# Optimization experiments

Hardware: AMD Instinct MI355X
Metric: run time of the kernel (lower is better)

Reference implementation:

```python
import jax, jax.numpy as jnp
import numpy as np

B, S, D, H, DF, L, V, MAXLEN = 8, 1024, 768, 12, 3072, 6, 32000, 2048
HD = D // H
EPS = 1e-5

def _pe(max_length, d_model):
    position = jnp.arange(max_length, dtype=jnp.float32)[:, None]
    i = jnp.arange(d_model, dtype=jnp.float32)[None, :]
    angles = position * (1.0 / jnp.power(10000.0, 2.0 * jnp.floor(i / 2.0) / d_model))
    pe = jnp.zeros((max_length, d_model), dtype=jnp.float32)
    pe = pe.at[:, 0::2].set(jnp.sin(angles[:, 0::2]))
    pe = pe.at[:, 1::2].set(jnp.cos(angles[:, 1::2]))
    return pe

def _layernorm(x, g, b):
    mu = jnp.mean(x, axis=-1, keepdims=True)
    var = jnp.mean((x - mu) ** 2, axis=-1, keepdims=True)
    return (x - mu) * jax.lax.rsqrt(var + EPS) * g + b

def setup_inputs() -> dict:
    key = jax.random.key(0)
    ks = jax.random.split(key, 16)
    s = 0.02
    emb = jax.random.normal(ks[0], (V, D), jnp.float32) * s
    emb = emb.at[0].set(0.0)  # padding_idx=0
    inp = {
        'input_ids': jax.random.randint(ks[1], (B, S), 0, V),
        'emb': emb,
        'pe': _pe(MAXLEN, D),
        'Wq': jax.random.normal(ks[2], (L, D, D), jnp.float32) * s,
        'bq': jnp.zeros((L, D), jnp.float32),
        'Wk': jax.random.normal(ks[3], (L, D, D), jnp.float32) * s,
        'bk': jnp.zeros((L, D), jnp.float32),
        'Wv': jax.random.normal(ks[4], (L, D, D), jnp.float32) * s,
        'bv': jnp.zeros((L, D), jnp.float32),
        'W1': jax.random.normal(ks[5], (L, DF, D), jnp.float32) * s,
        'b1': jnp.zeros((L, DF), jnp.float32),
        'W2': jax.random.normal(ks[6], (L, D, DF), jnp.float32) * s,
        'b2': jnp.zeros((L, D), jnp.float32),
        'ln1_g': jnp.ones((L, D), jnp.float32),
        'ln1_b': jnp.zeros((L, D), jnp.float32),
        'ln2_g': jnp.ones((L, D), jnp.float32),
        'ln2_b': jnp.zeros((L, D), jnp.float32),
    }
    return inp

def _mha(x, Wq, bq, Wk, bk, Wv, bv):
    b, s, _ = x.shape
    q = (x @ Wq.T + bq).reshape(b, H, s, HD)  # faithful to torch .view (no transpose)
    k = (x @ Wk.T + bk).reshape(b, H, s, HD)
    v = (x @ Wv.T + bv).reshape(b, H, s, HD)
    scores = jnp.einsum('bhqd,bhkd->bhqk', q, k) / (HD ** 0.5)
    att = jax.nn.softmax(scores, axis=-1)
    o = jnp.einsum('bhqk,bhkd->bhqd', att, v)
    return o.transpose(0, 2, 1, 3).reshape(b, s, D)

def reference(input_ids, emb, pe, Wq, bq, Wk, bk, Wv, bv, W1, b1, W2, b2, ln1_g, ln1_b, ln2_g, ln2_b):
    x = emb[input_ids] + pe[:input_ids.shape[1], :]
    # dropout is identity in eval mode
    for l in range(L):
        h1 = _mha(x, Wq[l], bq[l], Wk[l], bk[l], Wv[l], bv[l])
        y1 = _layernorm(x + h1, ln1_g[l], ln1_b[l])
        h2 = jax.nn.relu(y1 @ W1[l].T + b1[l]) @ W2[l].T + b2[l]
        x = _layernorm(y1 + h2, ln2_g[l], ln2_b[l])
    return x
```

## Files before the change

### kernel.cpp

```cpp
#include <hip/hip_runtime.h>


typedef _Float16 f16;
typedef _Float16 half4 __attribute__((ext_vector_type(4)));
typedef _Float16 half8 __attribute__((ext_vector_type(8)));
typedef float f32x4 __attribute__((ext_vector_type(4)));
typedef float f32x16 __attribute__((ext_vector_type(16)));

constexpr int Bn = 8, Sn = 1024, Dn = 768, Hn = 12, HDn = 64, DFn = 3072, Ln = 6;
constexpr int BS = Bn * Sn;

__device__ __forceinline__ void glds16(const f16* g, f16* l) {
  __builtin_amdgcn_global_load_lds(
      (const __attribute__((address_space(1))) unsigned int*)g,
      (__attribute__((address_space(3))) unsigned int*)l, 16, 0, 0);
}

__device__ __forceinline__ float ex2(float x) {
#if __has_builtin(__builtin_amdgcn_exp2f)
  return __builtin_amdgcn_exp2f(x);
#else
  return exp2f(x);
#endif
}

__global__ __launch_bounds__(256) void pack_qkv(
    const float* __restrict__ Wq, const float* __restrict__ Wk, const float* __restrict__ Wv,
    const float* __restrict__ bq, const float* __restrict__ bk, const float* __restrict__ bv,
    f16* __restrict__ Wo, float* __restrict__ bo) {
  const long per = (long)Dn * Dn;
  const long t = (long)blockIdx.x * 256 + threadIdx.x;
  const long totalW4 = (long)Ln * 3 * per / 4;
  if (t < totalW4) {
    const long i = t * 4;
    const int l = (int)(i / (3 * per));
    long rem = i - (long)l * 3 * per;
    const int which = (int)(rem / per);
    const long e = rem - (long)which * per;
    const float* s = (which == 0) ? Wq : ((which == 1) ? Wk : Wv);
    const float4 v = *(const float4*)&s[(long)l * per + e];
    half4 h = {(f16)v.x, (f16)v.y, (f16)v.z, (f16)v.w};
    *(half4*)&Wo[i] = h;
  }
  if (t < (long)Ln * 3 * Dn) {
    int l = (int)(t / (3 * Dn));
    int rem = (int)(t % (3 * Dn));
    int which = rem / Dn, c = rem % Dn;
    const float* s = (which == 0) ? bq : ((which == 1) ? bk : bv);
    bo[t] = s[l * Dn + c];
  }
}

__global__ __launch_bounds__(256) void f32_to_f16_k(
    const float* __restrict__ src, f16* __restrict__ dst, long n) {
  long i = ((long)blockIdx.x * 256 + threadIdx.x) * 4;
  if (i < n) {
    float4 v = *(const float4*)&src[i];
    half4 h = {(f16)v.x, (f16)v.y, (f16)v.z, (f16)v.w};
    *(half4*)&dst[i] = h;
  }
}

__global__ __launch_bounds__(256) void embed_k(
    const int* __restrict__ ids, const float* __restrict__ emb, const float* __restrict__ pe,
    float* __restrict__ Xf, f16* __restrict__ Xh) {
  const int row = blockIdx.x;
  const int s = row & (Sn - 1);
  const int id = ids[row];
  const size_t eb = (size_t)id * Dn, pb = (size_t)s * Dn, ob = (size_t)row * Dn;
  for (int c = threadIdx.x; c < Dn; c += 256) {
    float v = emb[eb + c] + pe[pb + c];
    Xf[ob + c] = v;
    Xh[ob + c] = (f16)v;
  }
}

template <int MODE>
__global__ __launch_bounds__(256) void gemm_bt(
    const f16* __restrict__ A, const f16* __restrict__ Bw, const float* __restrict__ bias,
    float* __restrict__ outF, f16* __restrict__ o0, f16* __restrict__ o1, f16* __restrict__ o2,
    int M, int N, int K, int lda) {
  const int m0 = blockIdx.x * 128;
  const int n0 = blockIdx.y * 128;
  const int tid = threadIdx.x;
  const int lane = tid & 63, wave = tid >> 6;
  const int wm = wave & 1, wn = wave >> 1;
  const int l15 = lane & 15, l4 = lane >> 4;

  constexpr int TILE = 128 * 32;
  __shared__ __align__(16) f16 As[2 * TILE];
  __shared__ __align__(16) f16 Bs[2 * TILE];

  const f32x4 z4 = {0.f, 0.f, 0.f, 0.f};
  f32x4 acc[4][4];
#pragma unroll
  for (int i = 0; i < 4; i++)
#pragma unroll
    for (int j = 0; j < 4; j++) acc[i][j] = z4;

  const int sRow = wave * 32 + (lane >> 2);
  const int sCol = (lane & 3) * 8;
  const int kz = (MODE == 4) ? ((int)blockIdx.z * K) : 0;
  const f16* gA = A + (size_t)(m0 + sRow) * lda + kz + sCol;
  const f16* gB = Bw + (size_t)(n0 + sRow) * lda + kz + sCol;
  f16* lA = &As[(wave * 32) * 32];
  f16* lB = &Bs[(wave * 32) * 32];
  const size_t rowStep = (size_t)16 * lda;

  auto stage = [&](int buf, int k0) {
    glds16(gA + k0, lA + buf * TILE);
    glds16(gA + k0 + rowStep, lA + buf * TILE + 16 * 32);
    glds16(gB + k0, lB + buf * TILE);
    glds16(gB + k0 + rowStep, lB + buf * TILE + 16 * 32);
  };

  stage(0, 0);
  __syncthreads();

  const int kr = 8 * l4;
  int cur = 0;
  for (int k0 = 0; k0 < K; k0 += 32) {
    if (k0 + 32 < K) stage(cur ^ 1, k0 + 32);
    half8 af[4], bfr[4];
#pragma unroll
    for (int i = 0; i < 4; i++)
      af[i] = *(const half8*)&As[cur * TILE + (wm * 64 + i * 16 + l15) * 32 + kr];
#pragma unroll
    for (int j = 0; j < 4; j++)
      bfr[j] = *(const half8*)&Bs[cur * TILE + (wn * 64 + j * 16 + l15) * 32 + kr];
#pragma unroll
    for (int i = 0; i < 4; i++)
#pragma unroll
      for (int j = 0; j < 4; j++)
        acc[i][j] = __builtin_amdgcn_mfma_f32_16x16x32_f16(af[i], bfr[j], acc[i][j], 0, 0, 0);
    __syncthreads();
    cur ^= 1;
  }

  const int colb = n0 + wn * 64;
  const int rowb = m0 + wm * 64;
#pragma unroll
  for (int j = 0; j < 4; j++) {
    const int col = colb + j * 16 + l15;
    const float bb = (MODE == 4) ? 0.f : bias[col];
#pragma unroll
    for (int i = 0; i < 4; i++) {
      const int rb = rowb + i * 16 + l4 * 4;
#pragma unroll
      for (int r = 0; r < 4; r++) {
        float v = acc[i][j][r] + bb;
        const int row = rb + r;
        if (MODE == 1) {
          v = fmaxf(v, 0.f);
          o0[(size_t)row * N + col] = (f16)v;
        } else if (MODE == 3) {
          const int sel = col / 768;
          const int cl = col - sel * 768;
          f16* op = (sel == 0) ? o0 : ((sel == 1) ? o1 : o2);
          op[(size_t)row * 768 + cl] = (f16)v;
        } else if (MODE == 4) {
          outF[((size_t)blockIdx.z * M + row) * N + col] = v;
        } else {
          o0[(size_t)row * N + col] = (f16)v;
        }
      }
    }
  }
}

__global__ __launch_bounds__(256, 3) void attn_k(
    const f16* __restrict__ Qg, const f16* __restrict__ Kg, const f16* __restrict__ Vg,
    float* __restrict__ O) {
  const int bh = blockIdx.x;
  const int q0 = blockIdx.y * 128;
  const int b = bh / Hn, h = bh - b * Hn;
  const size_t base = (size_t)b * (Sn * Dn) + (size_t)h * (Sn * HDn);
  const f16* Qh = Qg + base;
  const f16* Kh = Kg + base;
  const f16* Vh = Vg + base;

  const int tid = threadIdx.x, lane = tid & 63, wave = tid >> 6;
  const int l31 = lane & 31;
  const int hi = lane >> 5;

  __shared__ __align__(16) f16 Ks[64 * 72];
  __shared__ __align__(16) f16 Vt[64 * 72];

  const int qrow = q0 + wave * 32 + l31;
  half8 qf[4];
#pragma unroll
  for (int m = 0; m < 4; m++)
    qf[m] = *(const half8*)&Qh[(size_t)qrow * HDn + 16 * m + 8 * hi];

  f32x16 Oacc0, Oacc1;
#pragma unroll
  for (int i = 0; i < 16; i++) { Oacc0[i] = 0.f; Oacc1[i] = 0.f; }
  float mrow = -1e30f, lrow = 0.f;
  const float csc = 0.18033688011112042f;

  for (int kt = 0; kt < Sn / 64; ++kt) {
#pragma unroll
    for (int cc = 0; cc < 2; cc++) {
      const int c = tid + cc * 256;
      const int row = c >> 3, col = (c & 7) * 8;
      *(int4*)&Ks[row * 72 + col] = *(const int4*)&Kh[(size_t)(kt * 64 + row) * HDn + col];
    }
#pragma unroll
    for (int ee = 0; ee < 2; ee++) {
      const int e = tid + ee * 256;
      const int hd = e & 63, kpo = e >> 6;
      f16 tmp[8];
#pragma unroll
      for (int j = 0; j < 8; j++)
        tmp[j] = Vh[(size_t)(kt * 64 + kpo * 8 + j) * HDn + hd];
      *(int4*)&Vt[hd * 72 + kpo * 8] = *(const int4*)tmp;
    }
    __syncthreads();

    f32x16 s0, s1;
#pragma unroll
    for (int i = 0; i < 16; i++) { s0[i] = 0.f; s1[i] = 0.f; }
#pragma unroll
    for (int m = 0; m < 4; m++) {
      half8 k0 = *(const half8*)&Ks[l31 * 72 + 16 * m + 8 * hi];
      half8 k1 = *(const half8*)&Ks[(32 + l31) * 72 + 16 * m + 8 * hi];
      s0 = __builtin_amdgcn_mfma_f32_32x32x16_f16(k0, qf[m], s0, 0, 0, 0);
      s1 = __builtin_amdgcn_mfma_f32_32x32x16_f16(k1, qf[m], s1, 0, 0, 0);
    }

    float t8[8];
#pragma unroll
    for (int i = 0; i < 8; i++)
      t8[i] = fmaxf(fmaxf(s0[i], s0[i + 8]), fmaxf(s1[i], s1[i + 8]));
#pragma unroll
    for (int i = 0; i < 4; i++) t8[i] = fmaxf(t8[i], t8[i + 4]);
    float mx = fmaxf(fmaxf(t8[0], t8[1]), fmaxf(t8[2], t8[3]));
    mx = fmaxf(mx, __shfl_xor(mx, 32));
    const float M = fmaxf(mrow, mx * csc);
    const float alpha = ex2(mrow - M);

#pragma unroll
    for (int i = 0; i < 16; i++) {
      s0[i] = ex2(fmaf(s0[i], csc, -M));
      s1[i] = ex2(fmaf(s1[i], csc, -M));
    }
    float r0 = 0.f, r1 = 0.f, r2 = 0.f, r3 = 0.f;
#pragma unroll
    for (int i = 0; i < 16; i += 4) {
      r0 += s0[i]; r1 += s0[i + 1]; r2 += s0[i + 2]; r3 += s0[i + 3];
      r0 += s1[i]; r1 += s1[i + 1]; r2 += s1[i + 2]; r3 += s1[i + 3];
    }
    float rsum = (r0 + r1) + (r2 + r3);
    rsum += __shfl_xor(rsum, 32);
    lrow = lrow * alpha + rsum;
    mrow = M;
#pragma unroll
    for (int i = 0; i < 16; i++) { Oacc0[i] *= alpha; Oacc1[i] *= alpha; }

    unsigned pA[2][4], pB[2][4];
#pragma unroll
    for (int t = 0; t < 4; t++) {
      pA[0][t] = __builtin_bit_cast(unsigned, __builtin_amdgcn_cvt_pkrtz(s0[4 * t + 0], s0[4 * t + 1]));
      pB[0][t] = __builtin_bit_cast(unsigned, __builtin_amdgcn_cvt_pkrtz(s0[4 * t + 2], s0[4 * t + 3]));
      pA[1][t] = __builtin_bit_cast(unsigned, __builtin_amdgcn_cvt_pkrtz(s1[4 * t + 0], s1[4 * t + 1]));
      pB[1][t] = __builtin_bit_cast(unsigned, __builtin_amdgcn_cvt_pkrtz(s1[4 * t + 2], s1[4 * t + 3]));
    }

#pragma unroll
    for (int c = 0; c < 4; c++) {
      const int g = c >> 1, tt = 2 * (c & 1);
      const unsigned ownA = hi ? pA[g][tt + 1] : pA[g][tt];
      const unsigned ownB = hi ? pB[g][tt + 1] : pB[g][tt];
      const unsigned sndA = hi ? pA[g][tt] : pA[g][tt + 1];
      const unsigned sndB = hi ? pB[g][tt] : pB[g][tt + 1];
      const unsigned rA = (unsigned)__shfl_xor((int)sndA, 32);
      const unsigned rB = (unsigned)__shfl_xor((int)sndB, 32);
      int4 w;
      w.x = (int)(hi ? rA : ownA);
      w.y = (int)(hi ? rB : ownB);
      w.z = (int)(hi ? ownA : rA);
      w.w = (int)(hi ? ownB : rB);
      const half8 pf = __builtin_bit_cast(half8, w);
      const half8 v0 = *(const half8*)&Vt[l31 * 72 + 16 * c + 8 * hi];
      const half8 v1 = *(const half8*)&Vt[(32 + l31) * 72 + 16 * c + 8 * hi];
      Oacc0 = __builtin_amdgcn_mfma_f32_32x32x16_f16(v0, pf, Oacc0, 0, 0, 0);
      Oacc1 = __builtin_amdgcn_mfma_f32_32x32x16_f16(v1, pf, Oacc1, 0, 0, 0);
    }
    __syncthreads();
  }

  const float inv = 1.f / lrow;
  float* Orow = O + ((size_t)b * Sn + qrow) * Dn + h * HDn;
#pragma unroll
  for (int t = 0; t < 4; t++) {
    float4 o0, o1;
    o0.x = Oacc0[4 * t + 0] * inv; o0.y = Oacc0[4 * t + 1] * inv;
    o0.z = Oacc0[4 * t + 2] * inv; o0.w = Oacc0[4 * t + 3] * inv;
    o1.x = Oacc1[4 * t + 0] * inv; o1.y = Oacc1[4 * t + 1] * inv;
    o1.z = Oacc1[4 * t + 2] * inv; o1.w = Oacc1[4 * t + 3] * inv;
    *(float4*)&Orow[8 * t + 4 * hi] = o0;
    *(float4*)&Orow[32 + 8 * t + 4 * hi] = o1;
  }
}

__global__ __launch_bounds__(256) void add_ln(
    const float* __restrict__ Xi, const float* __restrict__ Hr,
    const float* __restrict__ g, const float* __restrict__ bt,
    float* __restrict__ Yf, f16* __restrict__ Yh) {
  const int row = blockIdx.x;
  const int tid = threadIdx.x;
  const size_t base = (size_t)row * Dn;
  float v0 = Xi[base + tid] + Hr[base + tid];
  float v1 = Xi[base + tid + 256] + Hr[base + tid + 256];
  float v2 = Xi[base + tid + 512] + Hr[base + tid + 512];

  __shared__ float red[8];
  float s = v0 + v1 + v2;
  for (int off = 32; off; off >>= 1) s += __shfl_down(s, off);
  const int wv = tid >> 6, ln = tid & 63;
  if (ln == 0) red[wv] = s;
  __syncthreads();
  if (tid == 0) red[4] = (red[0] + red[1] + red[2] + red[3]) * (1.f / Dn);
  __syncthreads();
  const float mu = red[4];
  const float d0 = v0 - mu, d1 = v1 - mu, d2 = v2 - mu;
  float vs = d0 * d0 + d1 * d1 + d2 * d2;
  for (int off = 32; off; off >>= 1) vs += __shfl_down(vs, off);
  if (ln == 0) red[wv] = vs;
  __syncthreads();
  if (tid == 0) red[5] = rsqrtf((red[0] + red[1] + red[2] + red[3]) * (1.f / Dn) + 1e-5f);
  __syncthreads();
  const float rs = red[5];
  float y0 = d0 * rs * g[tid] + bt[tid];
  float y1 = d1 * rs * g[tid + 256] + bt[tid + 256];
  float y2 = d2 * rs * g[tid + 512] + bt[tid + 512];
  Yf[base + tid] = y0;        Yh[base + tid] = (f16)y0;
  Yf[base + tid + 256] = y1;  Yh[base + tid + 256] = (f16)y1;
  Yf[base + tid + 512] = y2;  Yh[base + tid + 512] = (f16)y2;
}

__global__ __launch_bounds__(256) void add_ln_sk2(
    const float* __restrict__ Xi, const float* __restrict__ P,
    const float* __restrict__ b2, const float* __restrict__ g, const float* __restrict__ bt,
    float* __restrict__ Yf, f16* __restrict__ Yh) {
  const int row = blockIdx.x;
  const int tid = threadIdx.x;
  const size_t base = (size_t)row * Dn;
  const size_t cs = (size_t)BS * Dn;
  float v0 = Xi[base + tid]       + P[base + tid]       + P[cs + base + tid]       + b2[tid];
  float v1 = Xi[base + tid + 256] + P[base + tid + 256] + P[cs + base + tid + 256] + b2[tid + 256];
  float v2 = Xi[base + tid + 512] + P[base + tid + 512] + P[cs + base + tid + 512] + b2[tid + 512];

  __shared__ float red[8];
  float s = v0 + v1 + v2;
  for (int off = 32; off; off >>= 1) s += __shfl_down(s, off);
  const int wv = tid >> 6, ln = tid & 63;
  if (ln == 0) red[wv] = s;
  __syncthreads();
  if (tid == 0) red[4] = (red[0] + red[1] + red[2] + red[3]) * (1.f / Dn);
  __syncthreads();
  const float mu = red[4];
  const float d0 = v0 - mu, d1 = v1 - mu, d2 = v2 - mu;
  float vs = d0 * d0 + d1 * d1 + d2 * d2;
  for (int off = 32; off; off >>= 1) vs += __shfl_down(vs, off);
  if (ln == 0) red[wv] = vs;
  __syncthreads();
  if (tid == 0) red[5] = rsqrtf((red[0] + red[1] + red[2] + red[3]) * (1.f / Dn) + 1e-5f);
  __syncthreads();
  const float rs = red[5];
  float y0 = d0 * rs * g[tid] + bt[tid];
  float y1 = d1 * rs * g[tid + 256] + bt[tid + 256];
  float y2 = d2 * rs * g[tid + 512] + bt[tid + 512];
  Yf[base + tid] = y0;        Yh[base + tid] = (f16)y0;
  Yf[base + tid + 256] = y1;  Yh[base + tid + 256] = (f16)y1;
  Yf[base + tid + 512] = y2;  Yh[base + tid + 512] = (f16)y2;
}

extern "C" void kernel_launch(void* const* d_in, const int* in_sizes, int n_in,
                              void* d_out, int out_size, void* d_ws, size_t ws_size,
                              hipStream_t stream) {
  const int* ids  = (const int*)d_in[0];
  const float* emb = (const float*)d_in[1];
  const float* pe  = (const float*)d_in[2];
  const float* Wq  = (const float*)d_in[3];
  const float* bq  = (const float*)d_in[4];
  const float* Wk  = (const float*)d_in[5];
  const float* bk  = (const float*)d_in[6];
  const float* Wv  = (const float*)d_in[7];
  const float* bv  = (const float*)d_in[8];
  const float* W1  = (const float*)d_in[9];
  const float* b1  = (const float*)d_in[10];
  const float* W2  = (const float*)d_in[11];
  const float* b2  = (const float*)d_in[12];
  const float* g1  = (const float*)d_in[13];
  const float* be1 = (const float*)d_in[14];
  const float* g2  = (const float*)d_in[15];
  const float* be2 = (const float*)d_in[16];
  float* out = (float*)d_out;

  char* w = (char*)d_ws;
  auto alloc = [&](size_t bytes) {
    char* p = w;
    w += (bytes + 255) & ~(size_t)255;
    return p;
  };
  f16* Wqkv  = (f16*)alloc((size_t)Ln * 3 * Dn * Dn * 2);
  float* bqkv = (float*)alloc((size_t)Ln * 3 * Dn * 4);
  f16* W1h   = (f16*)alloc((size_t)Ln * DFn * Dn * 2);
  f16* W2h   = (f16*)alloc((size_t)Ln * Dn * DFn * 2);
  float* Xf  = (float*)alloc((size_t)BS * Dn * 4);
  f16* Xh    = (f16*)alloc((size_t)BS * Dn * 2);
  f16* Qh    = (f16*)alloc((size_t)BS * Dn * 2);
  f16* Kh    = (f16*)alloc((size_t)BS * Dn * 2);
  f16* Vh    = (f16*)alloc((size_t)BS * Dn * 2);
  float* Of  = (float*)alloc((size_t)BS * Dn * 4);
  float* Y1f = (float*)alloc((size_t)BS * Dn * 4);
  f16* Y1h   = (f16*)alloc((size_t)BS * Dn * 2);
  f16* F1h   = (f16*)alloc((size_t)BS * DFn * 2);

  float* Pf = (float*)Qh;

  {
    const long totalW4 = (long)Ln * 3 * Dn * Dn / 4;
    const int gw = (int)((totalW4 + 255) / 256);
    pack_qkv<<<gw, 256, 0, stream>>>(Wq, Wk, Wv, bq, bk, bv, Wqkv, bqkv);
    const long n1 = (long)Ln * DFn * Dn;
    const int gc = (int)(n1 / 4 / 256);
    f32_to_f16_k<<<gc, 256, 0, stream>>>(W1, W1h, n1);
    f32_to_f16_k<<<gc, 256, 0, stream>>>(W2, W2h, n1);
  }

  embed_k<<<BS, 256, 0, stream>>>(ids, emb, pe, Xf, Xh);

  for (int l = 0; l < Ln; ++l) {
    gemm_bt<3><<<dim3(BS / 128, (3 * Dn) / 128), 256, 0, stream>>>(
        Xh, Wqkv + (size_t)l * 3 * Dn * Dn, bqkv + l * 3 * Dn,
        nullptr, Qh, Kh, Vh, BS, 3 * Dn, Dn, Dn);

    attn_k<<<dim3(Bn * Hn, Sn / 128), 256, 0, stream>>>(Qh, Kh, Vh, Of);

    add_ln<<<BS, 256, 0, stream>>>(Xf, Of, g1 + l * Dn, be1 + l * Dn, Y1f, Y1h);

    gemm_bt<1><<<dim3(BS / 128, DFn / 128), 256, 0, stream>>>(
        Y1h, W1h + (size_t)l * DFn * Dn, b1 + l * DFn,
        nullptr, F1h, nullptr, nullptr, BS, DFn, Dn, Dn);

    gemm_bt<4><<<dim3(BS / 128, Dn / 128, 2), 256, 0, stream>>>(
        F1h, W2h + (size_t)l * Dn * DFn, nullptr,
        Pf, nullptr, nullptr, nullptr, BS, Dn, DFn / 2, DFn);

    float* dstF = (l == Ln - 1) ? out : Xf;
    add_ln_sk2<<<BS, 256, 0, stream>>>(Y1f, Pf, b2 + l * Dn,
                                       g2 + l * Dn, be2 + l * Dn, dstF, Xh);
  }
}
```

Baseline: 1.816 ms.

## Triple-buffer GEMM LDS staging with vmcnt-based waits and one barrier per step

Replaces the double-buffered K loop in the GEMM with a three-slot ring, prefetching two tiles ahead. Explicit s_waitcnt vmcnt waits for only the oldest tile's global-to-LDS loads, followed by a single barrier per iteration instead of a sync at the end of each step. The goal is to hide global load latency behind more MFMA work. In exchange it uses 50% more LDS, which may reduce occupancy, and it relies on a hand-set vmcnt count that must match the number of loads issued per stage.

```diff
diff --git a/kernel.cpp b/kernel.cpp
--- a/kernel.cpp
+++ b/kernel.cpp
@@ -87,9 +87,9 @@
   const int wm = wave & 1, wn = wave >> 1;
   const int l15 = lane & 15, l4 = lane >> 4;
 
-  constexpr int TILE = 128 * 32;
-  __shared__ __align__(16) f16 As[2 * TILE];
-  __shared__ __align__(16) f16 Bs[2 * TILE];
+  constexpr int SLOT = 128 * 32;
+  __shared__ __align__(16) f16 As[3 * SLOT];
+  __shared__ __align__(16) f16 Bs[3 * SLOT];
 
   const f32x4 z4 = {0.f, 0.f, 0.f, 0.f};
   f32x4 acc[4][4];
@@ -108,33 +108,45 @@
   const size_t rowStep = (size_t)16 * lda;
 
   auto stage = [&](int buf, int k0) {
-    glds16(gA + k0, lA + buf * TILE);
-    glds16(gA + k0 + rowStep, lA + buf * TILE + 16 * 32);
-    glds16(gB + k0, lB + buf * TILE);
-    glds16(gB + k0 + rowStep, lB + buf * TILE + 16 * 32);
+    glds16(gA + k0, lA + buf * SLOT);
+    glds16(gA + k0 + rowStep, lA + buf * SLOT + 16 * 32);
+    glds16(gB + k0, lB + buf * SLOT);
+    glds16(gB + k0 + rowStep, lB + buf * SLOT + 16 * 32);
   };
 
+  const int NT = K / 32;
   stage(0, 0);
-  __syncthreads();
+  stage(1, 32);
 
   const int kr = 8 * l4;
-  int cur = 0;
-  for (int k0 = 0; k0 < K; k0 += 32) {
-    if (k0 + 32 < K) stage(cur ^ 1, k0 + 32);
+  int cur = 0, nxt2 = 2;
+  for (int t = 0; t < NT; ++t) {
+    if (t + 1 < NT) {
+      asm volatile("s_waitcnt vmcnt(4)" ::: "memory");
+    } else {
+      asm volatile("s_waitcnt vmcnt(0)" ::: "memory");
+    }
+    __builtin_amdgcn_sched_barrier(0);
+    __builtin_amdgcn_s_barrier();
+    __builtin_amdgcn_sched_barrier(0);
+
+    if (t + 2 < NT) stage(nxt2, (t + 2) * 32);
+
     half8 af[4], bfr[4];
 #pragma unroll
     for (int i = 0; i < 4; i++)
-      af[i] = *(const half8*)&As[cur * TILE + (wm * 64 + i * 16 + l15) * 32 + kr];
+      af[i] = *(const half8*)&As[cur * SLOT + (wm * 64 + i * 16 + l15) * 32 + kr];
 #pragma unroll
     for (int j = 0; j < 4; j++)
-      bfr[j] = *(const half8*)&Bs[cur * TILE + (wn * 64 + j * 16 + l15) * 32 + kr];
+      bfr[j] = *(const half8*)&Bs[cur * SLOT + (wn * 64 + j * 16 + l15) * 32 + kr];
 #pragma unroll
     for (int i = 0; i < 4; i++)
 #pragma unroll
       for (int j = 0; j < 4; j++)
         acc[i][j] = __builtin_amdgcn_mfma_f32_16x16x32_f16(af[i], bfr[j], acc[i][j], 0, 0, 0);
-    __syncthreads();
-    cur ^= 1;
+
+    cur = (cur == 2) ? 0 : cur + 1;
+    nxt2 = (nxt2 == 2) ? 0 : nxt2 + 1;
   }
 
   const int colb = n0 + wn * 64;
```

After: 1.823 ms. Within noise of the previous version (+0.4%).
